# Kernel tuning notes

Hardware: AMD Instinct MI355X
Metric: run time of the kernel (lower is better)

Reference implementation:

```python
import jax, jax.numpy as jnp
import numpy as np

DIMS = (8, 8, 16, 16)   # 4D lattice, prod = 16384 sites
ND = len(DIMS)
N_IN = 4
N_OUT = 4
NC = 3
KERNEL_SIZE = 2
DILATION = 0
INIT_W = 1.0

W_IN = 2 * N_IN + 1                                  # 9
T_W = 2 * (N_IN * (KERNEL_SIZE - 1) * ND) + 1        # 33


def cconj(w):
    # swap matrix indices (axes 3,4) and negate imaginary part (last axis)
    wT = jnp.swapaxes(w, 3, 4)
    return wT * jnp.array([1.0, -1.0], dtype=w.dtype)


def complex_einsum(pattern, a, b, conj_a=1, conj_b=1):
    aR, aI = a[..., 0], conj_a * a[..., 1]
    bR, bI = b[..., 0], conj_b * b[..., 1]
    cR = jnp.einsum(pattern, aR, bR) - jnp.einsum(pattern, aI, bI)
    cI = jnp.einsum(pattern, aR, bI) + jnp.einsum(pattern, aI, bR)
    return jnp.stack((cR, cI), axis=-1)


def shift(a, axis, orientation):
    # dim 1 is flattened lattice; unflatten, roll along lattice axis, re-flatten
    o_s = a.shape
    n_s = (o_s[0],) + DIMS + o_s[2:]
    return jnp.roll(a.reshape(n_s), orientation, axis=axis + 1).reshape(o_s)


def transport(u, w, axis):
    # positive-orientation gauge transport: U w(x+mu) U^dagger
    ws = shift(w, axis, -1)
    ua = u[:, :, axis]                                 # [b, x, nc, nc, 2]
    wt = complex_einsum('bxij,bxwjk->bxwik', ua, ws)
    wt = complex_einsum('bxwij,bxkj->bxwik', wt, ua, conj_b=-1)
    return wt


def setup_inputs() -> dict:
    key = jax.random.key(0)
    k1, k2 = jax.random.split(key)
    n_sites = int(np.prod(DIMS))
    x = jax.random.normal(k1, (1, n_sites, ND + N_IN, NC, NC, 2), dtype=jnp.float32)
    std = INIT_W * np.sqrt(1.0 / (W_IN * T_W))
    weight = jax.random.normal(k2, (N_OUT, W_IN, T_W), dtype=jnp.float32) * std
    return {"x": x, "weight": weight}


def reference(x, weight):
    u, w = x[:, :, :ND], x[:, :, ND:]
    transported = []
    for axis in range(ND):
        wt = w
        for d in range(1, KERNEL_SIZE):
            for _ in range(DILATION + 1):
                wt = transport(u, wt, axis)
            transported.append(wt)
    t_w = jnp.concatenate(transported, axis=2)          # [b, x, n_in*(K-1)*ND, nc, nc, 2]

    w_full = jnp.concatenate([w, cconj(w)], axis=2)
    t_w_full = jnp.concatenate([t_w, cconj(t_w)], axis=2)

    # unit element channel
    unit = jnp.stack((jnp.eye(NC, dtype=x.dtype), jnp.zeros((NC, NC), dtype=x.dtype)), axis=-1)
    b, n_sites = x.shape[0], x.shape[1]
    unit_t = jnp.broadcast_to(unit[None, None, None], (b, n_sites, 1, NC, NC, 2))
    w_full = jnp.concatenate([w_full, unit_t], axis=2)       # [b, x, 9, nc, nc, 2]
    t_w_full = jnp.concatenate([t_w_full, unit_t], axis=2)   # [b, x, 33, nc, nc, 2]

    # bilinear gauge-covariant products, then weight contraction
    ww = complex_einsum('bxvij,bxwjk->bxvwik', w_full, t_w_full)  # [b, x, 9, 33, nc, nc, 2]
    w_out = jnp.einsum('uvw,bxvwijc->bxuijc', weight, ww)         # [b, x, n_out, nc, nc, 2]

    return jnp.concatenate([u, w_out], axis=2)
```

## Files before the change

### kernel.cpp

```cpp
#include <hip/hip_runtime.h>
#include <stdint.h>


typedef float v2f __attribute__((ext_vector_type(2)));

#define SPB 16
#define TPB 256
#define NSITES 16384
#define TS_TILE 10
#define TS2_SITE 164

#if defined(__has_builtin)
#if __has_builtin(__builtin_elementwise_fma)
#define HAVE_EW_FMA 1
#endif
#endif

__device__ __forceinline__ v2f pkfma(v2f a, v2f b, v2f c){
#ifdef HAVE_EW_FMA
    return __builtin_elementwise_fma(a, b, c);
#else
    v2f r; r.x = fmaf(a.x, b.x, c.x); r.y = fmaf(a.y, b.y, c.y); return r;
#endif
}
__device__ __forceinline__ v2f spl(float s){ return (v2f){s, s}; }
__device__ __forceinline__ v2f pn (float s){ return (v2f){s, -s}; }
__device__ __forceinline__ v2f np (float s){ return (v2f){-s, s}; }
__device__ __forceinline__ v2f swp(v2f a){ return __builtin_shufflevector(a, a, 1, 0); }
__device__ __forceinline__ v2f zero2(){ return (v2f){0.f, 0.f}; }

__device__ __forceinline__ int neigh(int s, int a){
    if (a == 3) return (s & ~15)        | ((s + 1)    & 15);
    if (a == 2) return (s & ~(15 << 4)) | ((s + 16)   & (15 << 4));
    if (a == 1) return (s & ~(7 << 8))  | ((s + 256)  & (7 << 8));
    return              (s & ~(7 << 11))| ((s + 2048) & (7 << 11));
}

__device__ __forceinline__ void load_tile(v2f* tc, const v2f* tp){
    const float4* tp4 = (const float4*)tp;
    float4 q0 = tp4[0], q1 = tp4[1], q2 = tp4[2], q3 = tp4[3];
    tc[0] = (v2f){q0.x, q0.y}; tc[1] = (v2f){q0.z, q0.w};
    tc[2] = (v2f){q1.x, q1.y}; tc[3] = (v2f){q1.z, q1.w};
    tc[4] = (v2f){q2.x, q2.y}; tc[5] = (v2f){q2.z, q2.w};
    tc[6] = (v2f){q3.x, q3.y}; tc[7] = (v2f){q3.z, q3.w};
    tc[8] = tp[8];
}

__global__ __launch_bounds__(TPB, 4)
void gcm_fused(const float* __restrict__ xp,
               const float* __restrict__ wgt,
               float* __restrict__ outp)
{
    __shared__ alignas(16) v2f    lt[SPB * TS2_SITE];
    __shared__ alignas(16) float4 wpk[16 * 17];
    __shared__ alignas(8)  float2 wpk8[4 * 17 + 16];
    const v2f* x2 = (const v2f*)xp;
    v2f* o2 = (v2f*)outp;

    const int tid = threadIdx.x;
    const int g   = tid & 3;
    const int u   = (tid >> 2) & 3;
    const int sl  = tid >> 4;
    const int s   = blockIdx.x * SPB + sl;

    v2f uc[9], wc[9];
    {
        const v2f* up = x2 + (s * 8 + u) * 9;
        #pragma unroll
        for (int e = 0; e < 9; e++) uc[e] = up[e];
    }
    {
        const int sn = neigh(s, u);
        const v2f* wp = x2 + (sn * 8 + 4 + g) * 9;
        #pragma unroll
        for (int e = 0; e < 9; e++) wc[e] = wp[e];
    }

    {
        const int u_ = tid >> 6, g_ = (tid >> 4) & 3, w_ = tid & 15;
        const float* wu_ = wgt + u_ * 297;
        wpk[(u_ * 4 + g_) * 17 + w_] =
            make_float4(wu_[g_ * 33 + w_],       wu_[g_ * 33 + 16 + w_],
                        wu_[(4 + g_) * 33 + w_], wu_[(4 + g_) * 33 + 16 + w_]);
        if (tid < 64){
            const int uu = tid >> 4, ww = tid & 15;
            const float* w8 = wgt + uu * 297 + 264;
            wpk8[uu * 17 + ww] = make_float2(w8[ww], w8[16 + ww]);
        }
    }
    __syncthreads();

    {
        v2f t1[9];
        #pragma unroll
        for (int r = 0; r < 3; r++){
            #pragma unroll
            for (int k = 0; k < 3; k++){
                v2f acc = zero2();
                #pragma unroll
                for (int j = 0; j < 3; j++){
                    v2f a_ = uc[r*3+j], b_ = wc[j*3+k];
                    acc = pkfma(spl(a_.x), b_, acc);
                    acc = pkfma(np(a_.y), swp(b_), acc);
                }
                t1[r*3+k] = acc;
            }
        }
        v2f tt[9];
        #pragma unroll
        for (int r = 0; r < 3; r++){
            #pragma unroll
            for (int k = 0; k < 3; k++){
                v2f acc = zero2();
                #pragma unroll
                for (int j = 0; j < 3; j++){
                    v2f a_ = t1[r*3+j], b_ = uc[k*3+j];
                    acc = pkfma(pn(a_.x), b_, acc);
                    acc = pkfma(spl(a_.y), swp(b_), acc);
                }
                tt[r*3+k] = acc;
            }
        }
        v2f* dst = &lt[sl * TS2_SITE + (u * 4 + g) * TS_TILE];
        float4* dst4 = (float4*)dst;
        dst4[0] = make_float4(tt[0].x, tt[0].y, tt[1].x, tt[1].y);
        dst4[1] = make_float4(tt[2].x, tt[2].y, tt[3].x, tt[3].y);
        dst4[2] = make_float4(tt[4].x, tt[4].y, tt[5].x, tt[5].y);
        dst4[3] = make_float4(tt[6].x, tt[6].y, tt[7].x, tt[7].y);
        dst[8] = tt[8];
    }

    if (g == 1){
        v2f* dst = o2 + (s * 8 + u) * 9;
        #pragma unroll
        for (int e = 0; e < 9; e++) dst[e] = uc[e];
    }

    asm volatile("s_waitcnt lgkmcnt(0)" ::: "memory");
    __builtin_amdgcn_sched_barrier(0);

    const float* wub = wgt + u * 297;
    const float wA32 = wub[g * 33 + 32];
    const float wB32 = wub[(4 + g) * 33 + 32];
    const float w832 = wub[296];

    v2f M1[9], M2[9];
    #pragma unroll
    for (int e = 0; e < 9; e++){ M1[e] = zero2(); M2[e] = zero2(); }

    const v2f* tbase = &lt[sl * TS2_SITE];
    const int ug17 = (u * 4 + g) * 17;

    #pragma unroll 2
    for (int w16 = 0; w16 < 16; w16++){
        v2f tc[9];
        load_tile(tc, tbase + w16 * TS_TILE);
        const float4 wq = wpk[ug17 + w16];
        const float a1 = wq.x, b1 = wq.y, a2 = wq.z, b2 = wq.w;
        #pragma unroll
        for (int i = 0; i < 3; i++){
            #pragma unroll
            for (int j = 0; j < 3; j++){
                const int e = i*3+j, eT = j*3+i;
                M1[e] = pkfma(spl(a1), tc[e],  M1[e]);
                M1[e] = pkfma(pn(b1),  tc[eT], M1[e]);
                M2[e] = pkfma(spl(a2), tc[e],  M2[e]);
                M2[e] = pkfma(pn(b2),  tc[eT], M2[e]);
            }
        }
    }

    v2f cc[9];
    #pragma unroll
    for (int e = 0; e < 9; e++) cc[e] = zero2();
    #pragma unroll 2
    for (int it = 0; it < 4; it++){
        const int w16 = g * 4 + it;
        v2f tc[9];
        load_tile(tc, tbase + w16 * TS_TILE);
        const float2 w8 = wpk8[u * 17 + w16];
        const float c8 = w8.x, d8 = w8.y;
        #pragma unroll
        for (int i = 0; i < 3; i++){
            #pragma unroll
            for (int j = 0; j < 3; j++){
                const int e = i*3+j, eT = j*3+i;
                cc[e] = pkfma(spl(c8), tc[e],  cc[e]);
                cc[e] = pkfma(pn(d8),  tc[eT], cc[e]);
            }
        }
    }

    {
        M1[0].x += wA32; M1[4].x += wA32; M1[8].x += wA32;
        M2[0].x += wB32; M2[4].x += wB32; M2[8].x += wB32;
        if (g == 0){
            cc[0].x += w832; cc[4].x += w832; cc[8].x += w832;
        }
    }

    v2f wg[9];
    {
        const v2f* wp = x2 + (s * 8 + 4 + g) * 9;
        #pragma unroll
        for (int e = 0; e < 9; e++) wg[e] = wp[e];
    }

    #pragma unroll
    for (int i = 0; i < 3; i++){
        #pragma unroll
        for (int k = 0; k < 3; k++){
            v2f acc = cc[i*3+k];
            #pragma unroll
            for (int j = 0; j < 3; j++){
                v2f a_ = wg[i*3+j];
                v2f m  = M1[j*3+k];
                acc = pkfma(spl(a_.x), m,      acc);
                acc = pkfma(np(a_.y),  swp(m), acc);
            }
            #pragma unroll
            for (int j = 0; j < 3; j++){
                v2f b_ = wg[j*3+i];
                v2f m  = M2[j*3+k];
                acc = pkfma(spl(b_.x), m,      acc);
                acc = pkfma(pn(b_.y),  swp(m), acc);
            }
            cc[i*3+k] = acc;
        }
    }

    #pragma unroll
    for (int e = 0; e < 9; e++){
        cc[e].x += __shfl_xor(cc[e].x, 1);
        cc[e].x += __shfl_xor(cc[e].x, 2);
        cc[e].y += __shfl_xor(cc[e].y, 1);
        cc[e].y += __shfl_xor(cc[e].y, 2);
    }
    if (g == 0){
        v2f* dst = o2 + (s * 8 + 4 + u) * 9;
        #pragma unroll
        for (int e = 0; e < 9; e++) dst[e] = cc[e];
    }
}

extern "C" void kernel_launch(void* const* d_in, const int* in_sizes, int n_in,
                              void* d_out, int out_size, void* d_ws, size_t ws_size,
                              hipStream_t stream)
{
    const float* x = (const float*)d_in[0];
    const float* w = (const float*)d_in[1];
    float* out = (float*)d_out;
    dim3 grid(NSITES / SPB);
    dim3 block(TPB);
    hipLaunchKernelGGL(gcm_fused, grid, block, 0, stream, x, w, out);
}
```

Baseline: 74.24 us.

## Halve threads per site so each thread handles two input channels

Each thread now processes two of the four input channels instead of one. It computes two transports and accumulates four M matrices plus the unit-channel term in a single loop over the 16 tiles. Each LDS tile load is reused across more accumulators, the separate second tile loop is removed, and the shuffle reduction drops to one step. Sites per block double to 32 with 8 threads per site, and launch bounds fall to 2 waves, which raises register pressure and may lower occupancy.

Result: no change. 75.60 us (+1.8%).

```diff
diff --git a/kernel.cpp b/kernel.cpp
--- a/kernel.cpp
+++ b/kernel.cpp
@@ -4,11 +4,12 @@
 
 typedef float v2f __attribute__((ext_vector_type(2)));
 
-#define SPB 16
+#define SPB 32
 #define TPB 256
 #define NSITES 16384
 #define TS_TILE 10
-#define TS2_SITE 164
+#define TS2_SITE 166
+#define WROW 49
 
 #if defined(__has_builtin)
 #if __has_builtin(__builtin_elementwise_fma)
@@ -34,6 +35,47 @@
     if (a == 2) return (s & ~(15 << 4)) | ((s + 16)   & (15 << 4));
     if (a == 1) return (s & ~(7 << 8))  | ((s + 256)  & (7 << 8));
     return              (s & ~(7 << 11))| ((s + 2048) & (7 << 11));
+}
+
+__device__ __forceinline__ void transport(const v2f* uc, const v2f* wc, v2f* tt){
+    v2f t1[9];
+    #pragma unroll
+    for (int r = 0; r < 3; r++){
+        #pragma unroll
+        for (int k = 0; k < 3; k++){
+            v2f acc = zero2();
+            #pragma unroll
+            for (int j = 0; j < 3; j++){
+                v2f a_ = uc[r*3+j], b_ = wc[j*3+k];
+                acc = pkfma(spl(a_.x), b_, acc);
+                acc = pkfma(np(a_.y), swp(b_), acc);
+            }
+            t1[r*3+k] = acc;
+        }
+    }
+    #pragma unroll
+    for (int r = 0; r < 3; r++){
+        #pragma unroll
+        for (int k = 0; k < 3; k++){
+            v2f acc = zero2();
+            #pragma unroll
+            for (int j = 0; j < 3; j++){
+                v2f a_ = t1[r*3+j], b_ = uc[k*3+j];
+                acc = pkfma(pn(a_.x), b_, acc);
+                acc = pkfma(spl(a_.y), swp(b_), acc);
+            }
+            tt[r*3+k] = acc;
+        }
+    }
+}
+
+__device__ __forceinline__ void store_tile(v2f* dst, const v2f* tt){
+    float4* dst4 = (float4*)dst;
+    dst4[0] = make_float4(tt[0].x, tt[0].y, tt[1].x, tt[1].y);
+    dst4[1] = make_float4(tt[2].x, tt[2].y, tt[3].x, tt[3].y);
+    dst4[2] = make_float4(tt[4].x, tt[4].y, tt[5].x, tt[5].y);
+    dst4[3] = make_float4(tt[6].x, tt[6].y, tt[7].x, tt[7].y);
+    dst[8] = tt[8];
 }
 
 __device__ __forceinline__ void load_tile(v2f* tc, const v2f* tp){
@@ -46,24 +88,25 @@
     tc[8] = tp[8];
 }
 
-__global__ __launch_bounds__(TPB, 4)
+__global__ __launch_bounds__(TPB, 2)
 void gcm_fused(const float* __restrict__ xp,
                const float* __restrict__ wgt,
                float* __restrict__ outp)
 {
     __shared__ alignas(16) v2f    lt[SPB * TS2_SITE];
-    __shared__ alignas(16) float4 wpk[16 * 17];
-    __shared__ alignas(8)  float2 wpk8[4 * 17 + 16];
+    __shared__ alignas(16) float4 wpk[8 * WROW];
     const v2f* x2 = (const v2f*)xp;
     v2f* o2 = (v2f*)outp;
 
     const int tid = threadIdx.x;
-    const int g   = tid & 3;
-    const int u   = (tid >> 2) & 3;
-    const int sl  = tid >> 4;
+    const int h   = tid & 1;
+    const int u   = (tid >> 1) & 3;
+    const int u2h = tid & 7;
+    const int sl  = tid >> 3;
     const int s   = blockIdx.x * SPB + sl;
-
-    v2f uc[9], wc[9];
+    const int g1  = 2 * h, g2 = 2 * h + 1;
+
+    v2f uc[9], wcA[9], wcB[9];
     {
         const v2f* up = x2 + (s * 8 + u) * 9;
         #pragma unroll
@@ -71,66 +114,39 @@
     }
     {
         const int sn = neigh(s, u);
-        const v2f* wp = x2 + (sn * 8 + 4 + g) * 9;
-        #pragma unroll
-        for (int e = 0; e < 9; e++) wc[e] = wp[e];
-    }
-
-    {
-        const int u_ = tid >> 6, g_ = (tid >> 4) & 3, w_ = tid & 15;
-        const float* wu_ = wgt + u_ * 297;
-        wpk[(u_ * 4 + g_) * 17 + w_] =
-            make_float4(wu_[g_ * 33 + w_],       wu_[g_ * 33 + 16 + w_],
-                        wu_[(4 + g_) * 33 + w_], wu_[(4 + g_) * 33 + 16 + w_]);
-        if (tid < 64){
-            const int uu = tid >> 4, ww = tid & 15;
-            const float* w8 = wgt + uu * 297 + 264;
-            wpk8[uu * 17 + ww] = make_float2(w8[ww], w8[16 + ww]);
-        }
+        const v2f* wp = x2 + (sn * 8 + 4 + g1) * 9;
+        #pragma unroll
+        for (int e = 0; e < 9; e++) wcA[e] = wp[e];
+        #pragma unroll
+        for (int e = 0; e < 9; e++) wcB[e] = wp[9 + e];
+    }
+
+    if (tid < 128){
+        const int u_ = tid >> 5, h_ = (tid >> 4) & 1, k = tid & 15;
+        const int w16 = (k < 8) ? 2 * k : 2 * k - 15;
+        const float* base = wgt + u_ * 297;
+        const int a1 = 2 * h_, a2 = 2 * h_ + 1;
+        float4 wA = make_float4(base[a1*33 + w16],     base[a1*33 + 16 + w16],
+                                base[a2*33 + w16],     base[a2*33 + 16 + w16]);
+        float4 wB = make_float4(base[(4+a1)*33 + w16], base[(4+a1)*33 + 16 + w16],
+                                base[(4+a2)*33 + w16], base[(4+a2)*33 + 16 + w16]);
+        const bool own = ((w16 >> 3) == h_);
+        float4 wC = make_float4(own ? base[264 + w16] : 0.f,
+                                own ? base[280 + w16] : 0.f, 0.f, 0.f);
+        float4* row = wpk + (u_ * 2 + h_) * WROW + k * 3;
+        row[0] = wA; row[1] = wB; row[2] = wC;
     }
     __syncthreads();
 
     {
-        v2f t1[9];
-        #pragma unroll
-        for (int r = 0; r < 3; r++){
-            #pragma unroll
-            for (int k = 0; k < 3; k++){
-                v2f acc = zero2();
-                #pragma unroll
-                for (int j = 0; j < 3; j++){
-                    v2f a_ = uc[r*3+j], b_ = wc[j*3+k];
-                    acc = pkfma(spl(a_.x), b_, acc);
-                    acc = pkfma(np(a_.y), swp(b_), acc);
-                }
-                t1[r*3+k] = acc;
-            }
-        }
         v2f tt[9];
-        #pragma unroll
-        for (int r = 0; r < 3; r++){
-            #pragma unroll
-            for (int k = 0; k < 3; k++){
-                v2f acc = zero2();
-                #pragma unroll
-                for (int j = 0; j < 3; j++){
-                    v2f a_ = t1[r*3+j], b_ = uc[k*3+j];
-                    acc = pkfma(pn(a_.x), b_, acc);
-                    acc = pkfma(spl(a_.y), swp(b_), acc);
-                }
-                tt[r*3+k] = acc;
-            }
-        }
-        v2f* dst = &lt[sl * TS2_SITE + (u * 4 + g) * TS_TILE];
-        float4* dst4 = (float4*)dst;
-        dst4[0] = make_float4(tt[0].x, tt[0].y, tt[1].x, tt[1].y);
-        dst4[1] = make_float4(tt[2].x, tt[2].y, tt[3].x, tt[3].y);
-        dst4[2] = make_float4(tt[4].x, tt[4].y, tt[5].x, tt[5].y);
-        dst4[3] = make_float4(tt[6].x, tt[6].y, tt[7].x, tt[7].y);
-        dst[8] = tt[8];
-    }
-
-    if (g == 1){
+        transport(uc, wcA, tt);
+        store_tile(&lt[sl * TS2_SITE + u2h * TS_TILE], tt);
+        transport(uc, wcB, tt);
+        store_tile(&lt[sl * TS2_SITE + (8 + u2h) * TS_TILE], tt);
+    }
+
+    if (h == 1){
         v2f* dst = o2 + (s * 8 + u) * 9;
         #pragma unroll
         for (int e = 0; e < 9; e++) dst[e] = uc[e];
@@ -139,73 +155,65 @@
     asm volatile("s_waitcnt lgkmcnt(0)" ::: "memory");
     __builtin_amdgcn_sched_barrier(0);
 
-    const float* wub = wgt + u * 297;
-    const float wA32 = wub[g * 33 + 32];
-    const float wB32 = wub[(4 + g) * 33 + 32];
-    const float w832 = wub[296];
-
-    v2f M1[9], M2[9];
-    #pragma unroll
-    for (int e = 0; e < 9; e++){ M1[e] = zero2(); M2[e] = zero2(); }
+    v2f M1a[9], M1b[9], M2a[9], M2b[9], cc[9];
+    #pragma unroll
+    for (int e = 0; e < 9; e++){
+        M1a[e] = zero2(); M1b[e] = zero2();
+        M2a[e] = zero2(); M2b[e] = zero2(); cc[e] = zero2();
+    }
 
     const v2f* tbase = &lt[sl * TS2_SITE];
-    const int ug17 = (u * 4 + g) * 17;
+    const float4* wrow = wpk + u2h * WROW;
 
     #pragma unroll 2
-    for (int w16 = 0; w16 < 16; w16++){
+    for (int k = 0; k < 16; k++){
         v2f tc[9];
-        load_tile(tc, tbase + w16 * TS_TILE);
-        const float4 wq = wpk[ug17 + w16];
-        const float a1 = wq.x, b1 = wq.y, a2 = wq.z, b2 = wq.w;
+        load_tile(tc, tbase + k * TS_TILE);
+        const float4 wA = wrow[k*3], wB = wrow[k*3 + 1];
+        const float2 w8 = *(const float2*)&wrow[k*3 + 2];
         #pragma unroll
         for (int i = 0; i < 3; i++){
             #pragma unroll
             for (int j = 0; j < 3; j++){
                 const int e = i*3+j, eT = j*3+i;
-                M1[e] = pkfma(spl(a1), tc[e],  M1[e]);
-                M1[e] = pkfma(pn(b1),  tc[eT], M1[e]);
-                M2[e] = pkfma(spl(a2), tc[e],  M2[e]);
-                M2[e] = pkfma(pn(b2),  tc[eT], M2[e]);
-            }
-        }
-    }
-
-    v2f cc[9];
-    #pragma unroll
-    for (int e = 0; e < 9; e++) cc[e] = zero2();
-    #pragma unroll 2
-    for (int it = 0; it < 4; it++){
-        const int w16 = g * 4 + it;
-        v2f tc[9];
-        load_tile(tc, tbase + w16 * TS_TILE);
-        const float2 w8 = wpk8[u * 17 + w16];
-        const float c8 = w8.x, d8 = w8.y;
-        #pragma unroll
-        for (int i = 0; i < 3; i++){
-            #pragma unroll
-            for (int j = 0; j < 3; j++){
-                const int e = i*3+j, eT = j*3+i;
-                cc[e] = pkfma(spl(c8), tc[e],  cc[e]);
-                cc[e] = pkfma(pn(d8),  tc[eT], cc[e]);
-            }
-        }
-    }
-
-    {
-        M1[0].x += wA32; M1[4].x += wA32; M1[8].x += wA32;
-        M2[0].x += wB32; M2[4].x += wB32; M2[8].x += wB32;
-        if (g == 0){
-            cc[0].x += w832; cc[4].x += w832; cc[8].x += w832;
-        }
-    }
-
-    v2f wg[9];
-    {
-        const v2f* wp = x2 + (s * 8 + 4 + g) * 9;
-        #pragma unroll
-        for (int e = 0; e < 9; e++) wg[e] = wp[e];
-    }
-
+                M1a[e] = pkfma(spl(wA.x), tc[e],  M1a[e]);
+                M1a[e] = pkfma(pn(wA.y),  tc[eT], M1a[e]);
+                M1b[e] = pkfma(spl(wA.z), tc[e],  M1b[e]);
+                M1b[e] = pkfma(pn(wA.w),  tc[eT], M1b[e]);
+                M2a[e] = pkfma(spl(wB.x), tc[e],  M2a[e]);
+                M2a[e] = pkfma(pn(wB.y),  tc[eT], M2a[e]);
+                M2b[e] = pkfma(spl(wB.z), tc[e],  M2b[e]);
+                M2b[e] = pkfma(pn(wB.w),  tc[eT], M2b[e]);
+                cc[e]  = pkfma(spl(w8.x), tc[e],  cc[e]);
+                cc[e]  = pkfma(pn(w8.y),  tc[eT], cc[e]);
+            }
+        }
+    }
+
+    {
+        const float* wub = wgt + u * 297;
+        const float iA = wub[g1 * 33 + 32];
+        const float iB = wub[g2 * 33 + 32];
+        const float iC = wub[(4 + g1) * 33 + 32];
+        const float iD = wub[(4 + g2) * 33 + 32];
+        M1a[0].x += iA; M1a[4].x += iA; M1a[8].x += iA;
+        M1b[0].x += iB; M1b[4].x += iB; M1b[8].x += iB;
+        M2a[0].x += iC; M2a[4].x += iC; M2a[8].x += iC;
+        M2b[0].x += iD; M2b[4].x += iD; M2b[8].x += iD;
+        if (h == 0){
+            const float i8 = wub[296];
+            cc[0].x += i8; cc[4].x += i8; cc[8].x += i8;
+        }
+    }
+
+    v2f wgA[9], wgB[9];
+    {
+        const v2f* wp = x2 + (s * 8 + 4 + g1) * 9;
+        #pragma unroll
+        for (int e = 0; e < 9; e++) wgA[e] = wp[e];
+        #pragma unroll
+        for (int e = 0; e < 9; e++) wgB[e] = wp[9 + e];
+    }
     #pragma unroll
     for (int i = 0; i < 3; i++){
         #pragma unroll
@@ -213,18 +221,28 @@
             v2f acc = cc[i*3+k];
             #pragma unroll
             for (int j = 0; j < 3; j++){
-                v2f a_ = wg[i*3+j];
-                v2f m  = M1[j*3+k];
+                v2f a_ = wgA[i*3+j], m = M1a[j*3+k];
                 acc = pkfma(spl(a_.x), m,      acc);
                 acc = pkfma(np(a_.y),  swp(m), acc);
             }
             #pragma unroll
             for (int j = 0; j < 3; j++){
-                v2f b_ = wg[j*3+i];
-                v2f m  = M2[j*3+k];
+                v2f a_ = wgB[i*3+j], m = M1b[j*3+k];
+                acc = pkfma(spl(a_.x), m,      acc);
+                acc = pkfma(np(a_.y),  swp(m), acc);
+            }
+            #pragma unroll
+            for (int j = 0; j < 3; j++){
+                v2f b_ = wgA[j*3+i], m = M2a[j*3+k];
                 acc = pkfma(spl(b_.x), m,      acc);
                 acc = pkfma(pn(b_.y),  swp(m), acc);
             }
+            #pragma unroll
+            for (int j = 0; j < 3; j++){
+                v2f b_ = wgB[j*3+i], m = M2b[j*3+k];
+                acc = pkfma(spl(b_.x), m,      acc);
+                acc = pkfma(pn(b_.y),  swp(m), acc);
+            }
             cc[i*3+k] = acc;
         }
     }
@@ -232,11 +250,9 @@
     #pragma unroll
     for (int e = 0; e < 9; e++){
         cc[e].x += __shfl_xor(cc[e].x, 1);
-        cc[e].x += __shfl_xor(cc[e].x, 2);
         cc[e].y += __shfl_xor(cc[e].y, 1);
-        cc[e].y += __shfl_xor(cc[e].y, 2);
-    }
-    if (g == 0){
+    }
+    if (h == 0){
         v2f* dst = o2 + (s * 8 + 4 + u) * 9;
         #pragma unroll
         for (int e = 0; e < 9; e++) dst[e] = cc[e];
```
